# Kernel tuning notes

Measured on AMD Instinct MI355X. Metric: run time of the kernel, lower is better.

## Reference

```python
import jax, jax.numpy as jnp
import numpy as np

BETA = 0.05
ALPHA = 0.01
CROSSCAM_EPOCH = 5
BG_KNN = 50
C, L, D = 8, 4096, 2048   # cameras, pseudo-classes per camera, feature dim
B = 256                   # batch, cam-sorted blocks of PERCAM samples
PERCAM = B // C


def setup_inputs() -> dict:
    key = jax.random.key(0)
    kf, km = jax.random.split(key)
    features = jax.random.normal(kf, (B, D), dtype=jnp.float32)
    # cams sorted in blocks; per-camera targets unique (PK-sampler style), spread over [0, L)
    cams = jnp.repeat(jnp.arange(C, dtype=jnp.int32), PERCAM)
    targets = jnp.tile(jnp.arange(PERCAM, dtype=jnp.int32) * (L // PERCAM), C)
    # dataset-level arrays: every camera observes all L labels -> identity class mapper,
    # concate_intra_class == tile(arange(L), C)
    all_img_cams = jnp.repeat(jnp.arange(C, dtype=jnp.int32), L)
    all_pseudo_label = jnp.tile(jnp.arange(L, dtype=jnp.int32), C)
    mem = jax.random.normal(km, (C, L, D), dtype=jnp.float32)
    init_intra_id_feat = mem / jnp.linalg.norm(mem, axis=-1, keepdims=True)
    return {"features": features, "targets": targets, "cams": cams,
            "all_pseudo_label": all_pseudo_label, "all_img_cams": all_img_cams,
            "init_intra_id_feat": init_intra_id_feat, "epoch": 10, "batch_ind": 0}


def _forward(features, init_intra_id_feat, targets, cams, epoch):
    Cn, Ln, Dn = init_intra_id_feat.shape
    Bn = features.shape[0]
    percam = Bn // Cn
    mem0 = jax.lax.stop_gradient(init_intra_id_feat)  # proxy memory buffer (detached in torch)
    # --- EMA memory update (torch.no_grad); (cam, target) pairs unique in batch ---
    f_sg = jax.lax.stop_gradient(features)
    old = mem0[cams, targets]                                   # [B, D] gather
    new = ALPHA * old + (1.0 - ALPHA) * f_sg
    new = new / jnp.linalg.norm(new, axis=1, keepdims=True)
    mem = mem0.at[cams, targets].set(new)                       # scatter update
    # --- per-camera proxy cross-entropy (cams are sorted blocks of `percam`) ---
    fn = features / jnp.linalg.norm(features, axis=1, keepdims=True)
    memn = mem / jnp.linalg.norm(mem, axis=-1, keepdims=True)   # rows already unit; faithful
    logits = jnp.einsum('cbd,cld->cbl', fn.reshape(Cn, percam, Dn), memn) / BETA
    lsm = jax.nn.log_softmax(logits, axis=-1)
    t = targets.reshape(Cn, percam)
    ce = -jnp.take_along_axis(lsm, t[..., None], axis=-1)[..., 0]   # [C, percam]
    loss = ce.mean(axis=1).sum()   # torch sums per-camera mean CE over unique batch cams
    # --- cross-camera associative loss (all_cam_feats built from pre-update memory) ---
    if epoch >= CROSSCAM_EPOCH:
        allf = mem0.reshape(Cn * Ln, Dn)
        allf = allf / jnp.linalg.norm(allf, axis=1, keepdims=True)
        sims = fn @ allf.T                                      # [B, C*L]
        # ori_asso_ind: label t appears once per camera block in concate_intra_class
        pos = targets[:, None] + jnp.arange(Cn)[None, :] * Ln   # [B, C]
        rows = jnp.arange(Bn)[:, None]
        pos_logits = sims[rows, pos] / BETA                     # [B, C]
        masked = sims.at[rows, pos].set(-10000.0)               # temp_sims masking
        topv, _ = jax.lax.top_k(masked, BG_KNN)                 # hardest negatives
        cat = jnp.concatenate([pos_logits, topv / BETA], axis=1)  # [B, C+BG_KNN]
        ls2 = jax.nn.log_softmax(cat, axis=1)
        per = -ls2[:, :Cn].sum(axis=1) / Cn                     # soft target 1/|ori| on positives
        loss = loss + 0.5 * per.reshape(Cn, percam).mean(axis=1).sum()
    return loss.reshape(1)


def reference(features, targets, cams, all_pseudo_label, all_img_cams,
              init_intra_id_feat, epoch, batch_ind):
    # all_pseudo_label / all_img_cams determine concate_intra_class; by construction
    # each camera holds all L labels, so positive indices are computed analytically.
    return _forward(features, init_intra_id_feat, targets, cams, epoch)
```

## Files before the change

### kernel.cpp

```cpp
#include <hip/hip_runtime.h>
#include <hip/hip_bf16.h>


#define Dn 2048
#define Ln 4096
#define Cn 8
#define Bn 256
#define NTOT 32768
#define INVB 20.0f
#define KNN 50

typedef __attribute__((ext_vector_type(8))) short short8;
typedef __attribute__((ext_vector_type(4))) float f32x4;

__device__ __forceinline__ unsigned short f2b(float f) {
    unsigned u = __float_as_uint(f);
    unsigned r = (u + 0x7FFFu + ((u >> 16) & 1u)) >> 16;
    return (unsigned short)r;
}

__device__ __forceinline__ unsigned pack2(float x, float y) {
    __hip_bfloat162 h = __float22bfloat162_rn(float2{x, y});
    unsigned u; __builtin_memcpy(&u, &h, 4); return u;
}

__global__ __launch_bounds__(256) void prep_kernel(
    const float* __restrict__ feat, const float* __restrict__ mem0,
    const int* __restrict__ targets, const int* __restrict__ cams,
    float* __restrict__ fn, float* __restrict__ nrows,
    unsigned short* __restrict__ fnb) {
    int i = blockIdx.x, tid = threadIdx.x;
    int c = cams[i], t = targets[i];
    const float* f = feat + (size_t)i * Dn;
    const float* o = mem0 + ((size_t)c * Ln + t) * Dn;
    float fv[8], nv[8];
    float s1 = 0.f, s2 = 0.f;
#pragma unroll
    for (int r = 0; r < 8; ++r) {
        int idx = tid + (r << 8);
        float a = f[idx], bb = o[idx];
        float n = 0.99f * a + 0.01f * bb;
        fv[r] = a; nv[r] = n;
        s1 += a * a; s2 += n * n;
    }
    __shared__ float red[2][4];
    for (int off = 32; off > 0; off >>= 1) {
        s1 += __shfl_down(s1, off);
        s2 += __shfl_down(s2, off);
    }
    int wv = tid >> 6;
    if ((tid & 63) == 0) { red[0][wv] = s1; red[1][wv] = s2; }
    __syncthreads();
    s1 = red[0][0] + red[0][1] + red[0][2] + red[0][3];
    s2 = red[1][0] + red[1][1] + red[1][2] + red[1][3];
    float r1 = 1.0f / sqrtf(s1), r2 = 1.0f / sqrtf(s2);
#pragma unroll
    for (int r = 0; r < 8; ++r) {
        int idx = tid + (r << 8);
        float a = fv[r] * r1;
        fn[(size_t)i * Dn + idx] = a;
        fnb[(size_t)i * Dn + idx] = f2b(a);
        nrows[(size_t)i * Dn + idx] = nv[r] * r2;
    }
}

#define GSTEP(KIT, CUR, NXT)                                                      \
  {                                                                               \
    if ((KIT) + 1 < 32) {                                                         \
      _Pragma("unroll") for (int mf = 0; mf < 4; ++mf)                            \
        _Pragma("unroll") for (int kb = 0; kb < 2; ++kb)                          \
          av[NXT][mf][kb] =                                                       \
            *(const short8*)&fnb[aoff[mf] + ((KIT) + 1) * 64 + kb * 32];          \
    }                                                                             \
    if ((KIT) + 2 < 32) {                                                         \
      _Pragma("unroll") for (int r = 0; r < 4; ++r)                               \
        rb[CUR][r] = *(const float4*)&mem0[boff[r] + ((KIT) + 2) * 64];           \
    }                                                                             \
    _Pragma("unroll") for (int kb = 0; kb < 2; ++kb) {                            \
      short8 bv[4];                                                               \
      _Pragma("unroll") for (int nf = 0; nf < 4; ++nf)                            \
        bv[nf] = *(const short8*)&lB[CUR][(nf * 16 + fr) * 72 + kb * 32 + fg * 8];\
      _Pragma("unroll") for (int mf = 0; mf < 4; ++mf)                            \
        _Pragma("unroll") for (int nf = 0; nf < 4; ++nf)                          \
          acc[mf][nf] = __builtin_amdgcn_mfma_f32_16x16x32_bf16(                  \
              av[CUR][mf][kb], bv[nf], acc[mf][nf], 0, 0, 0);                     \
    }                                                                             \
    if ((KIT) + 1 < 32) {                                                         \
      _Pragma("unroll") for (int r = 0; r < 4; ++r) {                             \
        float4 v = rb[NXT][r];                                                    \
        uint2 h; h.x = pack2(v.x, v.y); h.y = pack2(v.z, v.w);                    \
        *(uint2*)&lB[NXT][(r * 16 + btr) * 72 + btc * 4] = h;                     \
      }                                                                           \
    }                                                                             \
    __syncthreads();                                                              \
  }

__global__ __launch_bounds__(256, 2) void gemm_sims(
    const float* __restrict__ mem0, const unsigned short* __restrict__ fnb,
    float* __restrict__ sims) {
    __shared__ __align__(16) unsigned short lB[2][64 * 72];
    int tid = threadIdx.x;
    int n0 = blockIdx.x * 64;
    int lane = tid & 63, wv = tid >> 6;
    int fr = lane & 15, fg = lane >> 4;
    int btr = tid >> 4, btc = tid & 15;

    f32x4 acc[4][4];
#pragma unroll
    for (int a = 0; a < 4; ++a)
#pragma unroll
        for (int b = 0; b < 4; ++b)
#pragma unroll
            for (int k = 0; k < 4; ++k) acc[a][b][k] = 0.0f;

    size_t aoff[4], boff[4];
#pragma unroll
    for (int mf = 0; mf < 4; ++mf)
        aoff[mf] = (size_t)(wv * 64 + mf * 16 + fr) * Dn + fg * 8;
#pragma unroll
    for (int r = 0; r < 4; ++r)
        boff[r] = (size_t)(n0 + r * 16 + btr) * Dn + btc * 4;

    float4 rb[2][4];
    short8 av[2][4][2];
#pragma unroll
    for (int r = 0; r < 4; ++r) rb[0][r] = *(const float4*)&mem0[boff[r]];
#pragma unroll
    for (int r = 0; r < 4; ++r) rb[1][r] = *(const float4*)&mem0[boff[r] + 64];
#pragma unroll
    for (int mf = 0; mf < 4; ++mf)
#pragma unroll
        for (int kb = 0; kb < 2; ++kb)
            av[0][mf][kb] = *(const short8*)&fnb[aoff[mf] + kb * 32];
#pragma unroll
    for (int r = 0; r < 4; ++r) {
        float4 v = rb[0][r];
        uint2 h; h.x = pack2(v.x, v.y); h.y = pack2(v.z, v.w);
        *(uint2*)&lB[0][(r * 16 + btr) * 72 + btc * 4] = h;
    }
    __syncthreads();

    for (int k2 = 0; k2 < 16; ++k2) {
        GSTEP(2 * k2, 0, 1);
        GSTEP(2 * k2 + 1, 1, 0);
    }

    float* tbuf = (float*)lB;
    int row16 = lane & 15, seg = lane >> 4;
#pragma unroll
    for (int mf = 0; mf < 4; ++mf) {
#pragma unroll
        for (int nf = 0; nf < 4; ++nf)
#pragma unroll
            for (int r = 0; r < 4; ++r)
                tbuf[wv * 1088 + (fg * 4 + r) * 68 + nf * 16 + fr] = acc[mf][nf][r];
        __syncthreads();
#pragma unroll
        for (int q = 0; q < 4; ++q) {
            float4 v = *(float4*)&tbuf[wv * 1088 + row16 * 68 + seg * 16 + q * 4];
            int m = wv * 64 + mf * 16 + row16;
            *(float4*)&sims[(size_t)m * NTOT + n0 + seg * 16 + q * 4] = v;
        }
        __syncthreads();
    }
}

__global__ __launch_bounds__(256) void dots_kernel(
    const float* __restrict__ fn, const float* __restrict__ nrows,
    float* __restrict__ sdot_all) {
    int i = blockIdx.x, tid = threadIdx.x;
    int lane = tid & 63, wv = tid >> 6;
    int c = i >> 5;
    float f[32];
    const float* frp = fn + (size_t)i * Dn;
#pragma unroll
    for (int r = 0; r < 32; ++r) f[r] = frp[lane + (r << 6)];
    for (int jj = 0; jj < 8; ++jj) {
        int j = wv * 8 + jj;
        const float* nr = nrows + (size_t)(c * 32 + j) * Dn;
        float d = 0.f;
#pragma unroll
        for (int r = 0; r < 32; ++r) d += f[r] * nr[lane + (r << 6)];
        for (int o = 32; o > 0; o >>= 1) d += __shfl_down(d, o);
        if (lane == 0) sdot_all[i * 32 + j] = d;
    }
}

__global__ __launch_bounds__(256) void fused_kernel(
    const float* __restrict__ sims, const float* __restrict__ sdot_all,
    const int* __restrict__ targets, float* __restrict__ out) {
    __shared__ int hist[4][1024];
    __shared__ int ghist[64];
    __shared__ float buf[512];
    __shared__ int cnt, sh_bstar, sh_r, sh_total;
    __shared__ float wred[4], wmax4[4], wmin4[4], cesum[4];
    int i = blockIdx.x, tid = threadIdx.x;
    int wv = tid >> 6, lane = tid & 63;
    int t = targets[i], c = i >> 5, b = i & 31;
    const float* row = sims + (size_t)i * NTOT;

    float mx = -3e38f, mn = 3e38f, ce_p = 0.f;
    for (int q = 0; q < 128; ++q) {
        int j = tid + (q << 8);
        float v = row[j];
        if ((j >> 12) == c) ce_p += expf(v * INVB);
        if ((j & (Ln - 1)) != t) { mx = fmaxf(mx, v); mn = fminf(mn, v); }
    }
    for (int o = 32; o > 0; o >>= 1) {
        ce_p += __shfl_down(ce_p, o);
        mx = fmaxf(mx, __shfl_down(mx, o));
        mn = fminf(mn, __shfl_down(mn, o));
    }
    if (lane == 0) { cesum[wv] = ce_p; wmax4[wv] = mx; wmin4[wv] = mn; }
    __syncthreads();
    float hi = fmaxf(fmaxf(wmax4[0], wmax4[1]), fmaxf(wmax4[2], wmax4[3]));
    float lo = fminf(fminf(wmin4[0], wmin4[1]), fminf(wmin4[2], wmin4[3]));
    float rng = fmaxf(hi - lo, 1e-30f);

    float thr = 0.f, scale = 0.f;
    for (int att = 0; att < 3; ++att) {
        float frac = (att == 0) ? 0.25f : ((att == 1) ? 0.5f : 1.0001f);
        thr = hi - rng * frac;
        scale = 1023.0f / fmaxf(hi - thr, 1e-30f);
        for (int k = tid; k < 4096; k += 256) ((int*)hist)[k] = 0;
        __syncthreads();
        for (int q = 0; q < 128; ++q) {
            int j = tid + (q << 8);
            float v = row[j];
            if (v > thr && (j & (Ln - 1)) != t) {
                int bin = min(1023, (int)((v - thr) * scale));
                atomicAdd(&hist[wv][bin], 1);
            }
        }
        __syncthreads();
        for (int k = tid; k < 1024; k += 256)
            hist[0][k] = hist[0][k] + hist[1][k] + hist[2][k] + hist[3][k];
        __syncthreads();
        if (tid < 64) {
            int s = 0;
#pragma unroll
            for (int k = 0; k < 16; ++k) s += hist[0][tid * 16 + k];
            ghist[tid] = s;
        }
        __syncthreads();
        if (tid == 0) {
            int total = 0;
            for (int g = 0; g < 64; ++g) total += ghist[g];
            sh_total = total;
            if (total >= KNN) {
                int cum = 0, g = 63;
                for (; g > 0; --g) { if (cum + ghist[g] >= KNN) break; cum += ghist[g]; }
                int bb = g * 16 + 15;
                for (;; --bb) { int h = hist[0][bb]; if (cum + h >= KNN) break; cum += h; }
                sh_bstar = bb;
                sh_r = KNN - cum;
            }
        }
        __syncthreads();
        if (sh_total >= KNN) break;
        __syncthreads();
    }
    int bstar = sh_bstar;
    if (tid == 0) cnt = 0;
    __syncthreads();
    float lsum = 0.f;
    for (int q = 0; q < 128; ++q) {
        int j = tid + (q << 8);
        float v = row[j];
        if (v <= thr || (j & (Ln - 1)) == t) continue;
        int bin = min(1023, (int)((v - thr) * scale));
        if (bin > bstar) {
            lsum += expf(v * INVB);
        } else if (bin == bstar) {
            int p = atomicAdd(&cnt, 1);
            if (p < 512) buf[p] = v;
        }
    }
    for (int o = 32; o > 0; o >>= 1) lsum += __shfl_down(lsum, o);
    if (lane == 0) wred[wv] = lsum;
    __syncthreads();
    if (wv == 0) {
        int nb = min(cnt, 512);
        int r = sh_r;
        float bsum = 0.f;
        for (int s = 0; s < r; ++s) {
            float mv = -3e38f; int mi = 0;
            for (int k = lane; k < nb; k += 64) {
                float v = buf[k];
                if (v > mv) { mv = v; mi = k; }
            }
            for (int o = 32; o > 0; o >>= 1) {
                float ov = __shfl_down(mv, o);
                int oi = __shfl_down(mi, o);
                if (ov > mv) { mv = ov; mi = oi; }
            }
            mi = __shfl(mi, 0); mv = __shfl(mv, 0);
            if (lane == 0) { buf[mi] = -3e38f; bsum += expf(mv * INVB); }
            __builtin_amdgcn_wave_barrier();
        }
        if (lane == 0) {
            float S = wred[0] + wred[1] + wred[2] + wred[3] + bsum;
            float psum = 0.f, pls = 0.f;
#pragma unroll
            for (int c2 = 0; c2 < Cn; ++c2) {
                float pv = row[t + c2 * Ln] * INVB;
                psum += expf(pv);
                pls += pv;
            }
            S += psum;
            float per = logf(S) - pls * (1.0f / Cn);
            float sd = sdot_all[i * 32 + b];
            float Sce = cesum[0] + cesum[1] + cesum[2] + cesum[3]
                        - expf(row[(c << 12) + t] * INVB) + expf(sd * INVB);
            float ce = logf(Sce) - sd * INVB;
            atomicAdd(out, ce * (1.0f / 32.0f) + 0.5f * per * (1.0f / 32.0f));
        }
    }
}

extern "C" void kernel_launch(void* const* d_in, const int* in_sizes, int n_in,
                              void* d_out, int out_size, void* d_ws, size_t ws_size,
                              hipStream_t stream) {
    const float* feat    = (const float*)d_in[0];
    const int*   targets = (const int*)d_in[1];
    const int*   cams    = (const int*)d_in[2];
    const float* mem0    = (const float*)d_in[5];
    float* out = (float*)d_out;
    char* ws = (char*)d_ws;
    float*          fn    = (float*)(ws);
    float*          nrows = (float*)(ws + (size_t)(2 << 20));
    unsigned short* fnb   = (unsigned short*)(ws + (size_t)(4 << 20));
    float*          sdot  = (float*)(ws + (size_t)(6 << 20));
    float*          sims  = (float*)(ws + (size_t)(8 << 20));

    hipMemsetAsync(d_out, 0, (size_t)out_size * sizeof(float), stream);
    prep_kernel<<<Bn, 256, 0, stream>>>(feat, mem0, targets, cams, fn, nrows, fnb);
    gemm_sims<<<NTOT / 64, 256, 0, stream>>>(mem0, fnb, sims);
    dots_kernel<<<Bn, 256, 0, stream>>>(fn, nrows, sdot);
    fused_kernel<<<Bn, 256, 0, stream>>>(sims, sdot, targets, out);
}
```

Baseline: 505.5 us.

## Fold row min/max into GEMM epilogue and diagonal dot into prep

Removes dots_kernel, which computed all 32 same-camera dots per row although only the diagonal one is used. That single dot is now computed inside prep_kernel through shared memory, so the fp32 fn and nrows buffers are no longer written. The GEMM epilogue computes per-row max and min with atomics on order-preserving unsigned encodings, which removes the separate full pass over sims in fused_kernel. The cross-entropy exp-sum is folded into the first histogram pass. The max and min now include the positive positions, which can widen the histogram range and change how many threshold attempts run.

```diff
diff --git a/kernel.cpp b/kernel.cpp
--- a/kernel.cpp
+++ b/kernel.cpp
@@ -24,15 +24,28 @@
     unsigned u; __builtin_memcpy(&u, &h, 4); return u;
 }
 
+__device__ __forceinline__ unsigned fenc(float f) {
+    unsigned u = __float_as_uint(f);
+    return u ^ (((unsigned)((int)u >> 31)) | 0x80000000u);
+}
+__device__ __forceinline__ float fdec(unsigned e) {
+    unsigned mask = (e & 0x80000000u) ? 0x80000000u : 0xFFFFFFFFu;
+    return __uint_as_float(e ^ mask);
+}
+
 __global__ __launch_bounds__(256) void prep_kernel(
     const float* __restrict__ feat, const float* __restrict__ mem0,
     const int* __restrict__ targets, const int* __restrict__ cams,
-    float* __restrict__ fn, float* __restrict__ nrows,
-    unsigned short* __restrict__ fnb) {
+    unsigned short* __restrict__ fnb, float* __restrict__ sdot,
+    unsigned* __restrict__ rowmax, unsigned* __restrict__ rowmin) {
+    __shared__ float red[2][4];
+    __shared__ float lf[Dn];
+    __shared__ float lnr[Dn];
     int i = blockIdx.x, tid = threadIdx.x;
     int c = cams[i], t = targets[i];
     const float* f = feat + (size_t)i * Dn;
     const float* o = mem0 + ((size_t)c * Ln + t) * Dn;
+    if (tid == 0) { rowmax[i] = 0u; rowmin[i] = 0xFFFFFFFFu; }
     float fv[8], nv[8];
     float s1 = 0.f, s2 = 0.f;
 #pragma unroll
@@ -43,7 +56,6 @@
         fv[r] = a; nv[r] = n;
         s1 += a * a; s2 += n * n;
     }
-    __shared__ float red[2][4];
     for (int off = 32; off > 0; off >>= 1) {
         s1 += __shfl_down(s1, off);
         s2 += __shfl_down(s2, off);
@@ -58,9 +70,17 @@
     for (int r = 0; r < 8; ++r) {
         int idx = tid + (r << 8);
         float a = fv[r] * r1;
-        fn[(size_t)i * Dn + idx] = a;
         fnb[(size_t)i * Dn + idx] = f2b(a);
-        nrows[(size_t)i * Dn + idx] = nv[r] * r2;
+        lf[idx] = a;
+        lnr[idx] = nv[r] * r2;
+    }
+    __syncthreads();
+    if (tid < 64) {
+        float d = 0.f;
+#pragma unroll
+        for (int r = 0; r < 32; ++r) d += lf[tid + (r << 6)] * lnr[tid + (r << 6)];
+        for (int off = 32; off > 0; off >>= 1) d += __shfl_down(d, off);
+        if (tid == 0) sdot[i] = d;
     }
 }
 
@@ -97,7 +117,8 @@
 
 __global__ __launch_bounds__(256, 2) void gemm_sims(
     const float* __restrict__ mem0, const unsigned short* __restrict__ fnb,
-    float* __restrict__ sims) {
+    float* __restrict__ sims, unsigned* __restrict__ rowmax,
+    unsigned* __restrict__ rowmin) {
     __shared__ __align__(16) unsigned short lB[2][64 * 72];
     int tid = threadIdx.x;
     int n0 = blockIdx.x * 64;
@@ -155,69 +176,47 @@
             for (int r = 0; r < 4; ++r)
                 tbuf[wv * 1088 + (fg * 4 + r) * 68 + nf * 16 + fr] = acc[mf][nf][r];
         __syncthreads();
+        float mx = -3e38f, mn = 3e38f;
+        int m = wv * 64 + mf * 16 + row16;
 #pragma unroll
         for (int q = 0; q < 4; ++q) {
             float4 v = *(float4*)&tbuf[wv * 1088 + row16 * 68 + seg * 16 + q * 4];
-            int m = wv * 64 + mf * 16 + row16;
             *(float4*)&sims[(size_t)m * NTOT + n0 + seg * 16 + q * 4] = v;
-        }
-        __syncthreads();
-    }
-}
-
-__global__ __launch_bounds__(256) void dots_kernel(
-    const float* __restrict__ fn, const float* __restrict__ nrows,
-    float* __restrict__ sdot_all) {
-    int i = blockIdx.x, tid = threadIdx.x;
-    int lane = tid & 63, wv = tid >> 6;
-    int c = i >> 5;
-    float f[32];
-    const float* frp = fn + (size_t)i * Dn;
-#pragma unroll
-    for (int r = 0; r < 32; ++r) f[r] = frp[lane + (r << 6)];
-    for (int jj = 0; jj < 8; ++jj) {
-        int j = wv * 8 + jj;
-        const float* nr = nrows + (size_t)(c * 32 + j) * Dn;
-        float d = 0.f;
-#pragma unroll
-        for (int r = 0; r < 32; ++r) d += f[r] * nr[lane + (r << 6)];
-        for (int o = 32; o > 0; o >>= 1) d += __shfl_down(d, o);
-        if (lane == 0) sdot_all[i * 32 + j] = d;
+            mx = fmaxf(fmaxf(mx, fmaxf(v.x, v.y)), fmaxf(v.z, v.w));
+            mn = fminf(fminf(mn, fminf(v.x, v.y)), fminf(v.z, v.w));
+        }
+        mx = fmaxf(mx, __shfl_xor(mx, 16));
+        mx = fmaxf(mx, __shfl_xor(mx, 32));
+        mn = fminf(mn, __shfl_xor(mn, 16));
+        mn = fminf(mn, __shfl_xor(mn, 32));
+        if (seg == 0) {
+            atomicMax(&rowmax[m], fenc(mx));
+            atomicMin(&rowmin[m], fenc(mn));
+        }
+        __syncthreads();
     }
 }
 
 __global__ __launch_bounds__(256) void fused_kernel(
-    const float* __restrict__ sims, const float* __restrict__ sdot_all,
-    const int* __restrict__ targets, float* __restrict__ out) {
+    const float* __restrict__ sims, const float* __restrict__ sdot,
+    const int* __restrict__ targets, const unsigned* __restrict__ rowmax,
+    const unsigned* __restrict__ rowmin, float* __restrict__ out) {
     __shared__ int hist[4][1024];
     __shared__ int ghist[64];
     __shared__ float buf[512];
     __shared__ int cnt, sh_bstar, sh_r, sh_total;
-    __shared__ float wred[4], wmax4[4], wmin4[4], cesum[4];
+    __shared__ float wred[4], cesum[4];
     int i = blockIdx.x, tid = threadIdx.x;
     int wv = tid >> 6, lane = tid & 63;
-    int t = targets[i], c = i >> 5, b = i & 31;
+    int t = targets[i], c = i >> 5;
     const float* row = sims + (size_t)i * NTOT;
 
-    float mx = -3e38f, mn = 3e38f, ce_p = 0.f;
-    for (int q = 0; q < 128; ++q) {
-        int j = tid + (q << 8);
-        float v = row[j];
-        if ((j >> 12) == c) ce_p += expf(v * INVB);
-        if ((j & (Ln - 1)) != t) { mx = fmaxf(mx, v); mn = fminf(mn, v); }
-    }
-    for (int o = 32; o > 0; o >>= 1) {
-        ce_p += __shfl_down(ce_p, o);
-        mx = fmaxf(mx, __shfl_down(mx, o));
-        mn = fminf(mn, __shfl_down(mn, o));
-    }
-    if (lane == 0) { cesum[wv] = ce_p; wmax4[wv] = mx; wmin4[wv] = mn; }
-    __syncthreads();
-    float hi = fmaxf(fmaxf(wmax4[0], wmax4[1]), fmaxf(wmax4[2], wmax4[3]));
-    float lo = fminf(fminf(wmin4[0], wmin4[1]), fminf(wmin4[2], wmin4[3]));
+    float hi = fdec(rowmax[i]);
+    float lo = fdec(rowmin[i]);
     float rng = fmaxf(hi - lo, 1e-30f);
 
     float thr = 0.f, scale = 0.f;
+    float ce_p = 0.f;
     for (int att = 0; att < 3; ++att) {
         float frac = (att == 0) ? 0.25f : ((att == 1) ? 0.5f : 1.0001f);
         thr = hi - rng * frac;
@@ -227,6 +226,7 @@
         for (int q = 0; q < 128; ++q) {
             int j = tid + (q << 8);
             float v = row[j];
+            if (att == 0 && (j >> 12) == c) ce_p += expf(v * INVB);
             if (v > thr && (j & (Ln - 1)) != t) {
                 int bin = min(1023, (int)((v - thr) * scale));
                 atomicAdd(&hist[wv][bin], 1);
@@ -260,6 +260,8 @@
         if (sh_total >= KNN) break;
         __syncthreads();
     }
+    for (int o = 32; o > 0; o >>= 1) ce_p += __shfl_down(ce_p, o);
+    if (lane == 0) cesum[wv] = ce_p;
     int bstar = sh_bstar;
     if (tid == 0) cnt = 0;
     __syncthreads();
@@ -309,7 +311,7 @@
             }
             S += psum;
             float per = logf(S) - pls * (1.0f / Cn);
-            float sd = sdot_all[i * 32 + b];
+            float sd = sdot[i];
             float Sce = cesum[0] + cesum[1] + cesum[2] + cesum[3]
                         - expf(row[(c << 12) + t] * INVB) + expf(sd * INVB);
             float ce = logf(Sce) - sd * INVB;
@@ -327,15 +329,15 @@
     const float* mem0    = (const float*)d_in[5];
     float* out = (float*)d_out;
     char* ws = (char*)d_ws;
-    float*          fn    = (float*)(ws);
-    float*          nrows = (float*)(ws + (size_t)(2 << 20));
-    unsigned short* fnb   = (unsigned short*)(ws + (size_t)(4 << 20));
-    float*          sdot  = (float*)(ws + (size_t)(6 << 20));
-    float*          sims  = (float*)(ws + (size_t)(8 << 20));
+    unsigned short* fnb    = (unsigned short*)(ws);
+    float*          sdot   = (float*)(ws + (size_t)(1 << 20));
+    unsigned*       rowmax = (unsigned*)(ws + (size_t)(1 << 20) + 4096);
+    unsigned*       rowmin = (unsigned*)(ws + (size_t)(1 << 20) + 8192);
+    float*          sims   = (float*)(ws + (size_t)(8 << 20));
 
     hipMemsetAsync(d_out, 0, (size_t)out_size * sizeof(float), stream);
-    prep_kernel<<<Bn, 256, 0, stream>>>(feat, mem0, targets, cams, fn, nrows, fnb);
-    gemm_sims<<<NTOT / 64, 256, 0, stream>>>(mem0, fnb, sims);
-    dots_kernel<<<Bn, 256, 0, stream>>>(fn, nrows, sdot);
-    fused_kernel<<<Bn, 256, 0, stream>>>(sims, sdot, targets, out);
-}
+    prep_kernel<<<Bn, 256, 0, stream>>>(feat, mem0, targets, cams, fnb, sdot,
+                                        rowmax, rowmin);
+    gemm_sims<<<NTOT / 64, 256, 0, stream>>>(mem0, fnb, sims, rowmax, rowmin);
+    fused_kernel<<<Bn, 256, 0, stream>>>(sims, sdot, targets, rowmax, rowmin, out);
+}
```

Measured after the change: 488.6 us. -3.3%, faster.
